# Kernel optimization log

Measured on AMD Instinct MI355X. Metric: run time of the kernel, lower is better.

Reference implementation:

```python
import jax, jax.numpy as jnp
import numpy as np

N, E, G = 51200, 819200, 256            # nodes, directed edges, graphs
N2, A, E2 = 102400, 204800, 409600      # 2-sets, assignments, 2-set edges
D, L, NI2, NAF = 64, 5, 36, 40          # emb_dim, num_layer, num_i_2, num_atom_features
EPS = 1e-5


def _seg_sum(v, seg, n):
    return jax.ops.segment_sum(v, seg, num_segments=n)


def _seg_mean(v, seg, n):
    s = jax.ops.segment_sum(v, seg, num_segments=n)
    c = jax.ops.segment_sum(jnp.ones((v.shape[0],), v.dtype), seg, num_segments=n)
    return s / jnp.maximum(c, 1.0)[:, None]


def setup_inputs() -> dict:
    key = jax.random.key(0)
    ks = iter(jax.random.split(key, 64))
    nrm = lambda shape: jax.random.normal(next(ks), shape, jnp.float32) * 0.1
    x = jax.random.normal(next(ks), (N, NAF), jnp.float32)
    edge_index = jax.random.randint(next(ks), (2, E), 0, N, dtype=jnp.int32)
    edge_attr = jnp.stack([jax.random.randint(next(ks), (E,), 0, 4, dtype=jnp.int32),
                           jax.random.randint(next(ks), (E,), 0, 3, dtype=jnp.int32)], axis=1)
    batch = jnp.repeat(jnp.arange(G, dtype=jnp.int32), N // G)
    iso_type_2 = jax.nn.one_hot(jax.random.randint(next(ks), (N2,), 0, NI2), NI2, dtype=jnp.float32)
    edge_index_2 = jax.random.randint(next(ks), (2, E2), 0, N2, dtype=jnp.int32)
    assignment_index_2 = jnp.stack([jax.random.randint(next(ks), (A,), 0, N, dtype=jnp.int32),
                                    jnp.repeat(jnp.arange(N2, dtype=jnp.int32), 2)], axis=0)
    batch_2 = jnp.repeat(jnp.arange(G, dtype=jnp.int32), N2 // G)
    params = dict(
        emb_W=nrm((NAF, D)), emb_b=jnp.zeros((D,), jnp.float32),
        gin_W1=nrm((L, D, 2 * D)), gin_b1=jnp.zeros((L, 2 * D), jnp.float32),
        gin_W2=nrm((L, 2 * D, D)), gin_b2=jnp.zeros((L, D), jnp.float32),
        eemb1=nrm((L, 6, D)), eemb2=nrm((L, 3, D)),
        bn_gamma=jnp.ones((L, D), jnp.float32), bn_beta=jnp.zeros((L, D), jnp.float32),
        iso1_rel_W=nrm((D + NI2, D)), iso1_rel_b=jnp.zeros((D,), jnp.float32),
        iso1_root_W=nrm((D + NI2, D)),
        iso2_rel_W=nrm((D, D)), iso2_rel_b=jnp.zeros((D,), jnp.float32),
        iso2_root_W=nrm((D, D)),
        ro_W0=nrm((2 * D, D)), ro_b0=jnp.zeros((D,), jnp.float32),
        ro_W1=nrm((D, D // 2)), ro_b1=jnp.zeros((D // 2,), jnp.float32),
        ro_W2=nrm((D // 2, D // 4)), ro_b2=jnp.zeros((D // 4,), jnp.float32),
        last_W=nrm((D // 4, 1)), last_b=jnp.zeros((1,), jnp.float32),
    )
    return dict(x=x, edge_index=edge_index, edge_attr=edge_attr, batch=batch,
                iso_type_2=iso_type_2, edge_index_2=edge_index_2,
                assignment_index_2=assignment_index_2, batch_2=batch_2, **params)


def _forward(x, iso_type_2, emb_W, emb_b, gin_W1, gin_b1, gin_W2, gin_b2,
             eemb1, eemb2, bn_gamma, bn_beta,
             iso1_rel_W, iso1_rel_b, iso1_root_W, iso2_rel_W, iso2_rel_b, iso2_root_W,
             ro_W0, ro_b0, ro_W1, ro_b1, ro_W2, ro_b2, last_W, last_b,
             edge_index, edge_attr, batch, edge_index_2, assignment_index_2, batch_2):
    # --- GIN stack with edge-feature embeddings and self loops ---
    loop = jnp.arange(N, dtype=edge_index.dtype)
    src = jnp.concatenate([edge_index[0], loop])
    dst = jnp.concatenate([edge_index[1], loop])
    sl_attr = jnp.tile(jnp.array([[4, 0]], dtype=edge_attr.dtype), (N, 1))
    ea = jnp.concatenate([edge_attr, sl_attr], axis=0)  # [E+N, 2]

    h = jax.nn.relu(x @ emb_W + emb_b)  # x_embedding1
    for l in range(L):
        e = eemb1[l][ea[:, 0]] + eemb2[l][ea[:, 1]]      # [E+N, D]
        agg = _seg_sum(h[src] + e, dst, N)               # gather + scatter-add
        h2 = jax.nn.relu(agg @ gin_W1[l] + gin_b1[l]) @ gin_W2[l] + gin_b2[l]
        mu = jnp.mean(h2, axis=0)
        var = jnp.var(h2, axis=0)                        # biased, torch BN training mode
        h2 = (h2 - mu) / jnp.sqrt(var + EPS) * bn_gamma[l] + bn_beta[l]
        h = h2 if l == L - 1 else jax.nn.relu(h2)        # last layer: no ReLU (JK='last')
    node_rep = h

    # --- graph mean pool of node representation ---
    x1 = _seg_mean(node_rep, batch, G)                   # [G, D]

    # --- 2-set branch: avg_pool onto 2-sets, concat iso type, two GraphConvs ---
    xp = _seg_mean(node_rep[assignment_index_2[0]], assignment_index_2[1], N2)
    xp = jnp.concatenate([xp, iso_type_2], axis=1)       # [N2, D+NI2]

    def graph_conv(z, Wrel, brel, Wroot):
        agg = _seg_sum(z[edge_index_2[0]], edge_index_2[1], N2)
        return agg @ Wrel + brel + z @ Wroot

    xp = jax.nn.relu(graph_conv(xp, iso1_rel_W, iso1_rel_b, iso1_root_W))
    xp = jax.nn.relu(graph_conv(xp, iso2_rel_W, iso2_rel_b, iso2_root_W))
    x2 = _seg_mean(xp, batch_2, G)                       # [G, D]

    # --- readout MLP ---
    m = jnp.concatenate([x1, x2], axis=1)                # [G, 2D]
    m = jax.nn.relu(m @ ro_W0 + ro_b0)
    m = jax.nn.relu(m @ ro_W1 + ro_b1)
    m = jax.nn.relu(m @ ro_W2 + ro_b2)
    m = m @ last_W + last_b
    return m.reshape(-1)                                 # num_tasks == 1 -> flat [G]


def reference(x, edge_index, edge_attr, batch, iso_type_2, edge_index_2,
              assignment_index_2, batch_2, emb_W, emb_b, gin_W1, gin_b1, gin_W2,
              gin_b2, eemb1, eemb2, bn_gamma, bn_beta, iso1_rel_W, iso1_rel_b,
              iso1_root_W, iso2_rel_W, iso2_rel_b, iso2_root_W, ro_W0, ro_b0,
              ro_W1, ro_b1, ro_W2, ro_b2, last_W, last_b):
    return _forward(x, iso_type_2, emb_W, emb_b, gin_W1, gin_b1, gin_W2, gin_b2,
                    eemb1, eemb2, bn_gamma, bn_beta,
                    iso1_rel_W, iso1_rel_b, iso1_root_W, iso2_rel_W, iso2_rel_b,
                    iso2_root_W, ro_W0, ro_b0, ro_W1, ro_b1, ro_W2, ro_b2,
                    last_W, last_b, edge_index, edge_attr, batch, edge_index_2,
                    assignment_index_2, batch_2)
```

## Files before the change

kernel.cpp:

```cpp
#include <hip/hip_runtime.h>

#define NN   51200
#define EE   819200
#define GG   256
#define NN2  102400
#define AA   204800
#define EE2  409600
#define DD   64
#define LL   5

#define NB1  100
#define NB2  200
#define CAP1 10240
#define CAP2 3072

typedef __attribute__((ext_vector_type(8))) short bf16x8;
typedef __attribute__((ext_vector_type(4))) float f32x4;
typedef unsigned short ushort_t;

#define OFF_H      ((size_t)0)
#define OFF_AGG    ((size_t)13107200)
#define OFF_H2     ((size_t)26214400)
#define OFF_XP     ((size_t)39321600)
#define OFF_REC1   OFF_XP
#define OFF_REC2   ((size_t)47513600)
#define OFF_PERM   ((size_t)60293120)
#define OFF_YROOT  ((size_t)65536000)
#define OFF_OFFS1  ((size_t)91750400)
#define OFF_COL1   ((size_t)91955216)
#define OFF_OFFS2  ((size_t)95232016)
#define OFF_COL2   ((size_t)95641632)
#define OFF_CNT1   ((size_t)97280032)
#define OFF_BBASE  ((size_t)97282080)
#define OFF_CUR1   ((size_t)97484832)
#define OFF_STATS  ((size_t)98508832)
#define ZERO_BYTES ((size_t)1231360)
#define OFF_ISO    ((size_t)98511392)
#define OFF_M      ((size_t)98920992)
#define WS_NEEDED  ((size_t)99052064)

__device__ __forceinline__ int waveInclScan(int v, int lane) {
#pragma unroll
    for (int off = 1; off < 64; off <<= 1) {
        int t = __shfl_up(v, off, 64);
        if (lane >= off) v += t;
    }
    return v;
}

__device__ __forceinline__ void bsplit(float x, ushort_t& hi, ushort_t& lo) {
    union { float f; unsigned u; } a; a.f = x;
    unsigned hb = (a.u + 0x7FFFu + ((a.u >> 16) & 1u)) >> 16;
    union { unsigned u; float f; } h; h.u = hb << 16;
    float r = x - h.f;
    union { float f; unsigned u; } b; b.f = r;
    unsigned lb = (b.u + 0x7FFFu + ((b.u >> 16) & 1u)) >> 16;
    hi = (ushort_t)hb; lo = (ushort_t)lb;
}

__global__ __launch_bounds__(256) void kbA(const int* __restrict__ src1, const int* __restrict__ dst1,
                                           const int* __restrict__ ea,
                                           const int* __restrict__ src2, const int* __restrict__ dst2,
                                           int* __restrict__ bucketCnt,
                                           int2* __restrict__ rec1, int2* __restrict__ rec2) {
    __shared__ int lhist[256];
    __shared__ int lbase[256];
    int tid = threadIdx.x, b = blockIdx.x;
    lhist[tid] = 0;
    __syncthreads();
    if (b < 400) {
        int i = (b * 256 + tid) * 8;
        int4 d0 = *(const int4*)(dst1 + i);
        int4 d1 = *(const int4*)(dst1 + i + 4);
        int dst[8] = {d0.x, d0.y, d0.z, d0.w, d1.x, d1.y, d1.z, d1.w};
        int bin[8], lr[8];
#pragma unroll
        for (int j = 0; j < 8; ++j) {
            bin[j] = dst[j] >> 9;
            lr[j] = atomicAdd(&lhist[bin[j]], 1);
        }
        __syncthreads();
        if (tid < NB1) {
            int c = lhist[tid];
            lbase[tid] = c ? atomicAdd(&bucketCnt[tid], c) : 0;
        }
        __syncthreads();
        int4 s0 = *(const int4*)(src1 + i);
        int4 s1 = *(const int4*)(src1 + i + 4);
        int src[8] = {s0.x, s0.y, s0.z, s0.w, s1.x, s1.y, s1.z, s1.w};
        int4 e0 = *(const int4*)(ea + 2 * i);
        int4 e1 = *(const int4*)(ea + 2 * i + 4);
        int4 e2 = *(const int4*)(ea + 2 * i + 8);
        int4 e3 = *(const int4*)(ea + 2 * i + 12);
        int code[8] = {e0.x * 3 + e0.y, e0.z * 3 + e0.w, e1.x * 3 + e1.y, e1.z * 3 + e1.w,
                       e2.x * 3 + e2.y, e2.z * 3 + e2.w, e3.x * 3 + e3.y, e3.z * 3 + e3.w};
#pragma unroll
        for (int j = 0; j < 8; ++j) {
            int pos = bin[j] * CAP1 + lbase[bin[j]] + lr[j];
            rec1[pos] = make_int2(src[j] | (code[j] << 16), dst[j]);
        }
    } else {
        int i = ((b - 400) * 256 + tid) * 8;
        int4 d0 = *(const int4*)(dst2 + i);
        int4 d1 = *(const int4*)(dst2 + i + 4);
        int dst[8] = {d0.x, d0.y, d0.z, d0.w, d1.x, d1.y, d1.z, d1.w};
        int bin[8], lr[8];
#pragma unroll
        for (int j = 0; j < 8; ++j) {
            bin[j] = dst[j] >> 9;
            lr[j] = atomicAdd(&lhist[bin[j]], 1);
        }
        __syncthreads();
        if (tid < NB2) {
            int c = lhist[tid];
            lbase[tid] = c ? atomicAdd(&bucketCnt[NB1 + tid], c) : 0;
        }
        __syncthreads();
        int4 s0 = *(const int4*)(src2 + i);
        int4 s1 = *(const int4*)(src2 + i + 4);
        int src[8] = {s0.x, s0.y, s0.z, s0.w, s1.x, s1.y, s1.z, s1.w};
#pragma unroll
        for (int j = 0; j < 8; ++j) {
            int pos = bin[j] * CAP2 + lbase[bin[j]] + lr[j];
            rec2[pos] = make_int2(src[j], dst[j]);
        }
    }
}

__global__ void kbscan(const int* __restrict__ bucketCnt, int* __restrict__ bucketBase) {
    __shared__ int wsum[4];
    int tid = threadIdx.x, lane = tid & 63, wid = tid >> 6;
    int nb = blockIdx.x ? NB2 : NB1;
    const int* cnt = bucketCnt + (blockIdx.x ? NB1 : 0);
    int* base = bucketBase + (blockIdx.x ? NB1 : 0);
    int v = (tid < nb) ? cnt[tid] : 0;
    int incl = waveInclScan(v, lane);
    if (lane == 63) wsum[wid] = incl;
    __syncthreads();
    int woff = 0;
#pragma unroll
    for (int w = 0; w < 3; ++w) woff += (w < wid) ? wsum[w] : 0;
    if (tid < nb) base[tid] = woff + incl - v;
}

__global__ __launch_bounds__(256) void kbB(const int* __restrict__ bucketCnt,
                                           const int* __restrict__ bucketBase,
                                           const int2* __restrict__ rec1, const int2* __restrict__ rec2,
                                           int* __restrict__ offs1, int* __restrict__ col1,
                                           int* __restrict__ offs2, int* __restrict__ col2,
                                           int* __restrict__ dbin) {
    __shared__ int nh[512];
    __shared__ int ncur[512];
    __shared__ int wsum[4];
    __shared__ int dhist[64];
    int tid = threadIdx.x, b = blockIdx.x;
    bool g1 = b < NB1;
    const int2* rec = g1 ? (rec1 + (size_t)b * CAP1) : (rec2 + (size_t)(b - NB1) * CAP2);
    int cnt = bucketCnt[b];
    int base = bucketBase[b];
    int* offs = g1 ? offs1 : offs2;
    int* col = g1 ? col1 : col2;
    int nodeBase = g1 ? b * 512 : (b - NB1) * 512;
    nh[tid] = 0; nh[tid + 256] = 0;
    if (tid < 64) dhist[tid] = 0;
    __syncthreads();
    for (int e = tid; e < cnt; e += 256) {
        int2 r = rec[e];
        atomicAdd(&nh[r.y & 511], 1);
    }
    __syncthreads();
    int v0 = nh[2 * tid], v1 = nh[2 * tid + 1];
    int s = v0 + v1;
    int lane = tid & 63, wid = tid >> 6;
    int incl = waveInclScan(s, lane);
    if (lane == 63) wsum[wid] = incl;
    __syncthreads();
    int woff = 0;
#pragma unroll
    for (int w = 0; w < 3; ++w) woff += (w < wid) ? wsum[w] : 0;
    int excl = woff + incl - s;
    ncur[2 * tid] = excl;
    ncur[2 * tid + 1] = excl + v0;
    offs[nodeBase + 2 * tid] = base + excl;
    offs[nodeBase + 2 * tid + 1] = base + excl + v0;
    if (g1) {
        atomicAdd(&dhist[v0 < 63 ? v0 : 63], 1);
        atomicAdd(&dhist[v1 < 63 ? v1 : 63], 1);
    }
    __syncthreads();
    for (int e = tid; e < cnt; e += 256) {
        int2 r = rec[e];
        int node = r.y & 511;
        int slot = base + atomicAdd(&ncur[node], 1);
        col[slot] = r.x;
    }
    if (g1 && tid < 64 && dhist[tid]) atomicAdd(&dbin[tid], dhist[tid]);
    if (tid == 0) {
        if (b == NB1 - 1) offs1[NN] = EE;
        if (b == NB1 + NB2 - 1) offs2[NN2] = EE2;
    }
}

__global__ void kprepx(const float* __restrict__ x, const float* __restrict__ embW,
                       const float* __restrict__ embB, float* __restrict__ h,
                       const float* __restrict__ gW1, const float* __restrict__ gW2,
                       ushort_t* __restrict__ w1h, ushort_t* __restrict__ w1l,
                       ushort_t* __restrict__ w2h, ushort_t* __restrict__ w2l,
                       const float* __restrict__ iso, int* __restrict__ isoIdx) {
    int b = blockIdx.x;
    if (b < 12800) {
        int t = b * 256 + threadIdx.x;
        int n = t >> 6, d = t & 63;
        float acc = embB[d];
        const float* xr = x + n * 40;
#pragma unroll
        for (int k = 0; k < 40; ++k) acc = fmaf(xr[k], embW[k * 64 + d], acc);
        h[(size_t)n * 64 + d] = fmaxf(acc, 0.f);
    } else if (b < 12840) {
        int t = (b - 12800) * 256 + threadIdx.x;
        int lane = t & 63, frag = t >> 6;
        int c15 = lane & 15, q = lane >> 4;
        if (frag < 80) {
            int kt = frag & 1, nt = (frag >> 1) & 7, l = frag >> 4;
            const float* W = gW1 + l * 8192;
            ushort_t* oh = w1h + ((size_t)frag * 64 + lane) * 8;
            ushort_t* ol = w1l + ((size_t)frag * 64 + lane) * 8;
            int kb = kt * 32 + q * 8, colw = nt * 16 + c15;
#pragma unroll
            for (int j = 0; j < 8; ++j) {
                ushort_t hi, lo; bsplit(W[(kb + j) * 128 + colw], hi, lo);
                oh[j] = hi; ol[j] = lo;
            }
        } else if (frag < 160) {
            int f = frag - 80;
            int kt = f & 3, nt = (f >> 2) & 3, l = f >> 4;
            const float* W = gW2 + l * 8192;
            ushort_t* oh = w2h + ((size_t)f * 64 + lane) * 8;
            ushort_t* ol = w2l + ((size_t)f * 64 + lane) * 8;
            int kb = kt * 32 + q * 8, colw = nt * 16 + c15;
#pragma unroll
            for (int j = 0; j < 8; ++j) {
                ushort_t hi, lo; bsplit(W[(kb + j) * 64 + colw], hi, lo);
                oh[j] = hi; ol[j] = lo;
            }
        }
    } else {
        int j = (b - 12840) * 256 + threadIdx.x;
        const float4* r4 = (const float4*)(iso + (size_t)j * 36);
        int best = 0;
#pragma unroll
        for (int k = 0; k < 9; ++k) {
            float4 v = r4[k];
            if (v.x > 0.5f) best = 4 * k;
            if (v.y > 0.5f) best = 4 * k + 1;
            if (v.z > 0.5f) best = 4 * k + 2;
            if (v.w > 0.5f) best = 4 * k + 3;
        }
        isoIdx[j] = best;
    }
}

__global__ void kdegscan(const int* __restrict__ dbin, int* __restrict__ dstart) {
    int tid = threadIdx.x;
    int v = dbin[tid];
    int incl = waveInclScan(v, tid);
    dstart[tid] = incl - v;
}

__global__ __launch_bounds__(256) void kdegplace(const int* __restrict__ offs,
                                                 const int* __restrict__ dstart,
                                                 int* __restrict__ dcur,
                                                 int* __restrict__ perm) {
    __shared__ int lhist[64];
    __shared__ int lbase[64];
    int tid = threadIdx.x;
    if (tid < 64) lhist[tid] = 0;
    __syncthreads();
    int n = blockIdx.x * 256 + tid;
    int d = offs[n + 1] - offs[n]; d = d < 63 ? d : 63;
    int lr = atomicAdd(&lhist[d], 1);
    __syncthreads();
    if (tid < 64) {
        int c = lhist[tid];
        lbase[tid] = c ? atomicAdd(&dcur[tid], c) : 0;
    }
    __syncthreads();
    perm[dstart[d] + lbase[d] + lr] = n;
}

__global__ __launch_bounds__(256) void ktrans(float* __restrict__ h,
                                              const float* __restrict__ pst,
                                              const float* __restrict__ gamma,
                                              const float* __restrict__ beta) {
    __shared__ float sstat[128];
    __shared__ float sSC[64], sSH[64];
    int tid = threadIdx.x;
    if (tid < 128) {
        float s = 0.f;
        const float* p = pst + tid;
#pragma unroll
        for (int i = 0; i < 32; ++i) s += p[i * 128];
        sstat[tid] = s;
    }
    __syncthreads();
    if (tid < 64) {
        float mu = sstat[tid] * (1.f / NN);
        float var = sstat[64 + tid] * (1.f / NN) - mu * mu;
        float sc = gamma[tid] * rsqrtf(var + 1e-5f);
        sSC[tid] = sc; sSH[tid] = beta[tid] - mu * sc;
    }
    __syncthreads();
    int c = (tid & 15) * 4;
    float4 sc4 = *(const float4*)(sSC + c);
    float4 sh4 = *(const float4*)(sSH + c);
    float4* hp = (float4*)h;
    size_t base = (size_t)blockIdx.x * 1024 + tid;
#pragma unroll
    for (int r = 0; r < 4; ++r) {
        float4 v = hp[base + r * 256];
        v.x = fmaxf(fmaf(v.x, sc4.x, sh4.x), 0.f);
        v.y = fmaxf(fmaf(v.y, sc4.y, sh4.y), 0.f);
        v.z = fmaxf(fmaf(v.z, sc4.z, sh4.z), 0.f);
        v.w = fmaxf(fmaf(v.w, sc4.w, sh4.w), 0.f);
        hp[base + r * 256] = v;
    }
}

__global__ __launch_bounds__(256) void kglayer(
    const float* __restrict__ hin, float* __restrict__ hout,
    const int* __restrict__ perm,
    const int* __restrict__ offs, const int* __restrict__ col,
    const float* __restrict__ e1, const float* __restrict__ e2,
    const ushort_t* __restrict__ w1h, const ushort_t* __restrict__ w1l,
    const ushort_t* __restrict__ w2h, const ushort_t* __restrict__ w2l,
    const float* __restrict__ b1, const float* __restrict__ b2,
    float* __restrict__ pstout) {
    __shared__ float etab[13 * 64];
    __shared__ int sPerm[16];
    __shared__ float sMLP[16 * 132];
    float* sA = sMLP;
    float* sH = sMLP;
    int tid = threadIdx.x;
    if (tid < 16) sPerm[tid] = perm[blockIdx.x * 16 + tid];
    for (int idx = tid; idx < 13 * 64; idx += 256) {
        int ci = idx >> 6, dd = idx & 63;
        etab[idx] = e1[(ci / 3) * 64 + dd] + e2[(ci % 3) * 64 + dd];
    }
    __syncthreads();
    int lane = tid & 63, wv = tid >> 6;
    int c15 = lane & 15, q = lane >> 4;

    {
        int n = sPerm[wv * 4 + q];
        int s0 = offs[n], s1 = offs[n + 1];
        float4 sx = *(const float4*)(hin + (size_t)n * 64 + 4 * c15);
        float4 et = *(const float4*)(etab + 12 * 64 + 4 * c15);
        float a0 = sx.x + et.x, a1 = sx.y + et.y, a2 = sx.z + et.z, a3 = sx.w + et.w;
        int deg = s1 - s0;
        if (deg > 0) {
            const int* cp = col + s0;
            int nfull = deg >> 3, rem = deg & 7;
            int vv[8];
#pragma unroll
            for (int j = 0; j < 8; ++j) {
                int idx = j < deg ? j : deg - 1;
                vv[j] = cp[idx];
            }
            for (int it = 0; it < nfull; ++it) {
                float4 xv[8], tv[8];
#pragma unroll
                for (int j = 0; j < 8; ++j) {
                    xv[j] = *(const float4*)(hin + (size_t)(vv[j] & 0xFFFF) * 64 + 4 * c15);
                    tv[j] = *(const float4*)(etab + (vv[j] >> 16) * 64 + 4 * c15);
                }
                int e8 = (it + 1) * 8;
                bool more = e8 < deg;
                int nx[8];
                if (more) {
#pragma unroll
                    for (int j = 0; j < 8; ++j) {
                        int idx = e8 + j; idx = idx < deg ? idx : deg - 1;
                        nx[j] = cp[idx];
                    }
                }
#pragma unroll
                for (int j = 0; j < 8; ++j) {
                    a0 += xv[j].x + tv[j].x;
                    a1 += xv[j].y + tv[j].y;
                    a2 += xv[j].z + tv[j].z;
                    a3 += xv[j].w + tv[j].w;
                }
                if (more) {
#pragma unroll
                    for (int j = 0; j < 8; ++j) vv[j] = nx[j];
                }
            }
            if (rem) {
                float4 xv[8], tv[8];
#pragma unroll
                for (int j = 0; j < 8; ++j) {
                    xv[j] = *(const float4*)(hin + (size_t)(vv[j] & 0xFFFF) * 64 + 4 * c15);
                    tv[j] = *(const float4*)(etab + (vv[j] >> 16) * 64 + 4 * c15);
                }
#pragma unroll
                for (int j = 0; j < 8; ++j) {
                    float mm = (j < rem) ? 1.f : 0.f;
                    a0 = fmaf(xv[j].x + tv[j].x, mm, a0);
                    a1 = fmaf(xv[j].y + tv[j].y, mm, a1);
                    a2 = fmaf(xv[j].z + tv[j].z, mm, a2);
                    a3 = fmaf(xv[j].w + tv[j].w, mm, a3);
                }
            }
        }
        *(float4*)(sA + (wv * 4 + q) * 68 + 4 * c15) = make_float4(a0, a1, a2, a3);
    }
    __syncthreads();

    bf16x8 ah[2], al[2];
#pragma unroll
    for (int kt = 0; kt < 2; ++kt) {
        const float* p = sA + c15 * 68 + kt * 32 + q * 8;
        float4 x0 = *(const float4*)p;
        float4 x1 = *(const float4*)(p + 4);
        float xs[8] = {x0.x, x0.y, x0.z, x0.w, x1.x, x1.y, x1.z, x1.w};
#pragma unroll
        for (int j = 0; j < 8; ++j) {
            ushort_t hi, lo; bsplit(xs[j], hi, lo);
            ah[kt][j] = (short)hi; al[kt][j] = (short)lo;
        }
    }
    __syncthreads();

    f32x4 acc1[2];
#pragma unroll
    for (int j = 0; j < 2; ++j) { f32x4 z = {0.f, 0.f, 0.f, 0.f}; acc1[j] = z; }
#pragma unroll
    for (int kt = 0; kt < 2; ++kt) {
#pragma unroll
        for (int j = 0; j < 2; ++j) {
            int nt = 2 * wv + j;
            size_t fo = ((size_t)((nt * 2 + kt) * 64 + lane)) * 8;
            bf16x8 bh = *(const bf16x8*)(w1h + fo);
            bf16x8 bl = *(const bf16x8*)(w1l + fo);
            acc1[j] = __builtin_amdgcn_mfma_f32_16x16x32_bf16(ah[kt], bh, acc1[j], 0, 0, 0);
            acc1[j] = __builtin_amdgcn_mfma_f32_16x16x32_bf16(al[kt], bh, acc1[j], 0, 0, 0);
            acc1[j] = __builtin_amdgcn_mfma_f32_16x16x32_bf16(ah[kt], bl, acc1[j], 0, 0, 0);
        }
    }
#pragma unroll
    for (int j = 0; j < 2; ++j) {
        int nt = 2 * wv + j;
        float bias = b1[nt * 16 + c15];
#pragma unroll
        for (int rg = 0; rg < 4; ++rg)
            sH[(4 * q + rg) * 132 + nt * 16 + c15] = fmaxf(acc1[j][rg] + bias, 0.f);
    }
    __syncthreads();

    f32x4 acc2 = {0.f, 0.f, 0.f, 0.f};
#pragma unroll
    for (int kt = 0; kt < 4; ++kt) {
        const float* p = sH + c15 * 132 + kt * 32 + q * 8;
        float4 x0 = *(const float4*)p;
        float4 x1 = *(const float4*)(p + 4);
        float xs[8] = {x0.x, x0.y, x0.z, x0.w, x1.x, x1.y, x1.z, x1.w};
        bf16x8 a2h, a2l;
#pragma unroll
        for (int j = 0; j < 8; ++j) {
            ushort_t hi, lo; bsplit(xs[j], hi, lo);
            a2h[j] = (short)hi; a2l[j] = (short)lo;
        }
        size_t fo = ((size_t)((wv * 4 + kt) * 64 + lane)) * 8;
        bf16x8 bh = *(const bf16x8*)(w2h + fo);
        bf16x8 bl = *(const bf16x8*)(w2l + fo);
        acc2 = __builtin_amdgcn_mfma_f32_16x16x32_bf16(a2h, bh, acc2, 0, 0, 0);
        acc2 = __builtin_amdgcn_mfma_f32_16x16x32_bf16(a2l, bh, acc2, 0, 0, 0);
        acc2 = __builtin_amdgcn_mfma_f32_16x16x32_bf16(a2h, bl, acc2, 0, 0, 0);
    }
    {
        float bias = b2[wv * 16 + c15];
        float s = 0.f, s2 = 0.f;
#pragma unroll
        for (int rg = 0; rg < 4; ++rg) {
            float v = acc2[rg] + bias;
            hout[(size_t)sPerm[4 * q + rg] * 64 + wv * 16 + c15] = v;
            s += v; s2 += v * v;
        }
        s += __shfl_xor(s, 16, 64);  s += __shfl_xor(s, 32, 64);
        s2 += __shfl_xor(s2, 16, 64); s2 += __shfl_xor(s2, 32, 64);
        if (q == 0) {
            float* ps = pstout + (size_t)(blockIdx.x & 31) * 128;
            atomicAdd(&ps[wv * 16 + c15], s);
            atomicAdd(&ps[64 + wv * 16 + c15], s2);
        }
    }
}

template <int FIRST>
__global__ __launch_bounds__(256) void kgcmm(const float* __restrict__ X,
                                             const float* __restrict__ Wrel,
                                             const float* __restrict__ Wroot,
                                             const float* __restrict__ WrelIso,
                                             const float* __restrict__ WrootIso,
                                             const int* __restrict__ isoIdx,
                                             float* __restrict__ Yrel,
                                             float* __restrict__ Yroot,
                                             const float* __restrict__ pst,
                                             const float* __restrict__ g4,
                                             const float* __restrict__ b4,
                                             const int* __restrict__ a0g,
                                             const float* __restrict__ h2src) {
    __shared__ float sX[64 * 65];
    __shared__ float sR[64 * 64];
    __shared__ float sT[64 * 64];
    __shared__ float sstat[128];
    __shared__ float sSC[64], sSH[64];
    int tid = threadIdx.x, blk = blockIdx.x;
    if (FIRST && tid < 128) {
        float s = 0.f;
        const float* p = pst + tid;
#pragma unroll
        for (int i = 0; i < 32; ++i) s += p[i * 128];
        sstat[tid] = s;
    }
#pragma unroll
    for (int i = tid; i < 1024; i += 256) {
        ((float4*)sR)[i] = ((const float4*)Wrel)[i];
        ((float4*)sT)[i] = ((const float4*)Wroot)[i];
    }
    __syncthreads();
    if (FIRST && tid < 64) {
        float mu = sstat[tid] * (1.f / NN);
        float var = sstat[64 + tid] * (1.f / NN) - mu * mu;
        float sc = g4[tid] * rsqrtf(var + 1e-5f);
        sSC[tid] = sc;
        sSH[tid] = b4[tid] - mu * sc;
    }
    __syncthreads();
#pragma unroll
    for (int i = tid; i < 1024; i += 256) {
        int row = i >> 4, c = (i & 15) << 2;
        float4 v;
        if (FIRST) {
            int grow = blk * 64 + row;
            int na = a0g[2 * grow], nb = a0g[2 * grow + 1];
            float4 va = *(const float4*)(h2src + (size_t)na * 64 + c);
            float4 vb = *(const float4*)(h2src + (size_t)nb * 64 + c);
            v.x = 0.5f * (va.x + vb.x); v.y = 0.5f * (va.y + vb.y);
            v.z = 0.5f * (va.z + vb.z); v.w = 0.5f * (va.w + vb.w);
            v.x = fmaf(v.x, sSC[c], sSH[c]);
            v.y = fmaf(v.y, sSC[c + 1], sSH[c + 1]);
            v.z = fmaf(v.z, sSC[c + 2], sSH[c + 2]);
            v.w = fmaf(v.w, sSC[c + 3], sSH[c + 3]);
        } else {
            v = ((const float4*)(X + (size_t)blk * 4096))[i];
        }
        float* p = sX + row * 65 + c;
        p[0] = v.x; p[1] = v.y; p[2] = v.z; p[3] = v.w;
    }
    __syncthreads();
    int tm = tid >> 4, tn = tid & 15;
    float aR[4][4], aT[4][4];
#pragma unroll
    for (int r = 0; r < 4; ++r)
#pragma unroll
        for (int c = 0; c < 4; ++c) { aR[r][c] = 0.f; aT[r][c] = 0.f; }
    const float* xrow = sX + tm * 4 * 65;
#pragma unroll 4
    for (int k = 0; k < 64; ++k) {
        float a0 = xrow[k], a1 = xrow[65 + k], a2 = xrow[130 + k], a3 = xrow[195 + k];
        float4 br = *(const float4*)(sR + k * 64 + tn * 4);
        float4 bt = *(const float4*)(sT + k * 64 + tn * 4);
        float rb[4] = {br.x, br.y, br.z, br.w};
        float tb[4] = {bt.x, bt.y, bt.z, bt.w};
#pragma unroll
        for (int c = 0; c < 4; ++c) {
            aR[0][c] = fmaf(a0, rb[c], aR[0][c]); aR[1][c] = fmaf(a1, rb[c], aR[1][c]);
            aR[2][c] = fmaf(a2, rb[c], aR[2][c]); aR[3][c] = fmaf(a3, rb[c], aR[3][c]);
            aT[0][c] = fmaf(a0, tb[c], aT[0][c]); aT[1][c] = fmaf(a1, tb[c], aT[1][c]);
            aT[2][c] = fmaf(a2, tb[c], aT[2][c]); aT[3][c] = fmaf(a3, tb[c], aT[3][c]);
        }
    }
#pragma unroll
    for (int r = 0; r < 4; ++r) {
        int row = blk * 64 + tm * 4 + r;
        float4 vr = make_float4(aR[r][0], aR[r][1], aR[r][2], aR[r][3]);
        float4 vt = make_float4(aT[r][0], aT[r][1], aT[r][2], aT[r][3]);
        if (FIRST) {
            int ii = isoIdx[row];
            float4 er = *(const float4*)(WrelIso + (size_t)ii * 64 + tn * 4);
            float4 et = *(const float4*)(WrootIso + (size_t)ii * 64 + tn * 4);
            vr.x += er.x; vr.y += er.y; vr.z += er.z; vr.w += er.w;
            vt.x += et.x; vt.y += et.y; vt.z += et.z; vt.w += et.w;
        }
        *(float4*)(Yrel + (size_t)row * 64 + tn * 4) = vr;
        *(float4*)(Yroot + (size_t)row * 64 + tn * 4) = vt;
    }
}

__global__ void kgather2(const float* __restrict__ yrel, const float* __restrict__ yroot,
                         const float* __restrict__ brel, const int* __restrict__ offs,
                         const int* __restrict__ col, float* __restrict__ out) {
    int t = blockIdx.x * 256 + threadIdx.x;
    int j = t >> 4, c = t & 15;
    int s0 = offs[j], s1 = offs[j + 1];
    float4 rt = *(const float4*)(yroot + (size_t)j * 64 + 4 * c);
    float4 bb = *(const float4*)(brel + 4 * c);
    float a0 = rt.x + bb.x, a1 = rt.y + bb.y, a2 = rt.z + bb.z, a3 = rt.w + bb.w;
    if (s0 < s1) {
        int vv[4];
#pragma unroll
        for (int jj = 0; jj < 4; ++jj) {
            int idx = s0 + jj; idx = idx < s1 ? idx : s1 - 1;
            vv[jj] = col[idx];
        }
        int e = s0;
        while (true) {
            int ne = e + 4;
            bool more = ne < s1;
            float4 xs[4];
#pragma unroll
            for (int jj = 0; jj < 4; ++jj)
                xs[jj] = *(const float4*)(yrel + (size_t)vv[jj] * 64 + 4 * c);
            int nx[4];
            if (more) {
#pragma unroll
                for (int jj = 0; jj < 4; ++jj) {
                    int idx = ne + jj; idx = idx < s1 ? idx : s1 - 1;
                    nx[jj] = col[idx];
                }
            }
#pragma unroll
            for (int jj = 0; jj < 4; ++jj) {
                float mm = (e + jj < s1) ? 1.f : 0.f;
                a0 = fmaf(xs[jj].x, mm, a0);
                a1 = fmaf(xs[jj].y, mm, a1);
                a2 = fmaf(xs[jj].z, mm, a2);
                a3 = fmaf(xs[jj].w, mm, a3);
            }
            if (!more) break;
            e = ne;
#pragma unroll
            for (int jj = 0; jj < 4; ++jj) vv[jj] = nx[jj];
        }
    }
    *(float4*)(out + (size_t)j * 64 + 4 * c) =
        make_float4(fmaxf(a0, 0.f), fmaxf(a1, 0.f), fmaxf(a2, 0.f), fmaxf(a3, 0.f));
}

__global__ void kpoolg(const float* __restrict__ h2, const float* __restrict__ xp2,
                       const float* __restrict__ pst, const float* __restrict__ g4,
                       const float* __restrict__ b4, float* __restrict__ m) {
    __shared__ float sstat[128];
    __shared__ float red[4][64];
    int g = blockIdx.x, tid = threadIdx.x;
    if (tid < 128) {
        float s = 0.f;
        const float* p = pst + tid;
#pragma unroll
        for (int i = 0; i < 32; ++i) s += p[i * 128];
        sstat[tid] = s;
    }
    int wid = tid >> 6, d = tid & 63;
    float s1 = 0.f;
    for (int i = wid; i < 200; i += 4) s1 += h2[((size_t)g * 200 + i) * 64 + d];
    red[wid][d] = s1;
    __syncthreads();
    if (wid == 0) {
        float mean = (red[0][d] + red[1][d] + red[2][d] + red[3][d]) * (1.f / 200.f);
        float mu = sstat[d] * (1.f / NN);
        float var = sstat[64 + d] * (1.f / NN) - mu * mu;
        float sc = g4[d] * rsqrtf(var + 1e-5f);
        m[g * 128 + d] = fmaf(mean, sc, b4[d] - mu * sc);
    }
    __syncthreads();
    float s2 = 0.f;
    for (int i = wid; i < 400; i += 4) s2 += xp2[((size_t)g * 400 + i) * 64 + d];
    red[wid][d] = s2;
    __syncthreads();
    if (wid == 0) m[g * 128 + 64 + d] = (red[0][d] + red[1][d] + red[2][d] + red[3][d]) * (1.f / 400.f);
}

__global__ void kread(const float* __restrict__ m, const float* __restrict__ W0,
                      const float* __restrict__ b0, const float* __restrict__ W1,
                      const float* __restrict__ b1, const float* __restrict__ W2,
                      const float* __restrict__ b2, const float* __restrict__ lw,
                      const float* __restrict__ lb, float* __restrict__ out) {
    __shared__ float s0[64], s1[32], s2[16];
    int g = blockIdx.x, d = threadIdx.x;
    const float* mr = m + g * 128;
    float t = b0[d];
    for (int k = 0; k < 128; ++k) t = fmaf(mr[k], W0[k * 64 + d], t);
    s0[d] = fmaxf(t, 0.f);
    __syncthreads();
    if (d < 32) {
        float u = b1[d];
        for (int k = 0; k < 64; ++k) u = fmaf(s0[k], W1[k * 32 + d], u);
        s1[d] = fmaxf(u, 0.f);
    }
    __syncthreads();
    if (d < 16) {
        float u = b2[d];
        for (int k = 0; k < 32; ++k) u = fmaf(s1[k], W2[k * 16 + d], u);
        s2[d] = fmaxf(u, 0.f);
    }
    __syncthreads();
    if (d == 0) {
        float u = lb[0];
        for (int k = 0; k < 16; ++k) u = fmaf(s2[k], lw[k], u);
        out[g] = u;
    }
}

extern "C" void kernel_launch(void* const* d_in, const int* in_sizes, int n_in,
                              void* d_out, int out_size, void* d_ws, size_t ws_size,
                              hipStream_t stream) {
    if (ws_size < WS_NEEDED) return;

    const float* x    = (const float*)d_in[0];
    const int*   ei   = (const int*)d_in[1];
    const int*   ea   = (const int*)d_in[2];
    const float* iso  = (const float*)d_in[4];
    const int*   ei2  = (const int*)d_in[5];
    const int*   ai2  = (const int*)d_in[6];
    const float* embW = (const float*)d_in[8];
    const float* embB = (const float*)d_in[9];
    const float* gW1  = (const float*)d_in[10];
    const float* gB1  = (const float*)d_in[11];
    const float* gW2  = (const float*)d_in[12];
    const float* gB2  = (const float*)d_in[13];
    const float* ee1  = (const float*)d_in[14];
    const float* ee2  = (const float*)d_in[15];
    const float* bng  = (const float*)d_in[16];
    const float* bnb  = (const float*)d_in[17];
    const float* i1rW = (const float*)d_in[18];
    const float* i1rB = (const float*)d_in[19];
    const float* i1tW = (const float*)d_in[20];
    const float* i2rW = (const float*)d_in[21];
    const float* i2rB = (const float*)d_in[22];
    const float* i2tW = (const float*)d_in[23];
    const float* roW0 = (const float*)d_in[24];
    const float* roB0 = (const float*)d_in[25];
    const float* roW1 = (const float*)d_in[26];
    const float* roB1 = (const float*)d_in[27];
    const float* roW2 = (const float*)d_in[28];
    const float* roB2 = (const float*)d_in[29];
    const float* lW   = (const float*)d_in[30];
    const float* lB   = (const float*)d_in[31];
    float* out = (float*)d_out;

    char* ws = (char*)d_ws;
    float* h      = (float*)(ws + OFF_H);
    float* hB     = (float*)(ws + OFF_AGG);
    float* hA     = (float*)(ws + OFF_H2);
    float* h2     = hA;
    float* xp     = (float*)(ws + OFF_XP);
    float* yrel   = (float*)(ws + OFF_H);
    float* yroot  = (float*)(ws + OFF_YROOT);
    int* offs1    = (int*)(ws + OFF_OFFS1);
    int* col1     = (int*)(ws + OFF_COL1);
    int* offs2    = (int*)(ws + OFF_OFFS2);
    int* col2     = (int*)(ws + OFF_COL2);
    int* isoIdx   = (int*)(ws + OFF_ISO);
    float* mbuf   = (float*)(ws + OFF_M);
    ushort_t* w1h = (ushort_t*)(ws + OFF_YROOT);
    ushort_t* w1l = (ushort_t*)(ws + OFF_YROOT + 81920);
    ushort_t* w2h = (ushort_t*)(ws + OFF_YROOT + 163840);
    ushort_t* w2l = (ushort_t*)(ws + OFF_YROOT + 245760);
    float* pstat2 = (float*)(ws + OFF_CUR1);
    int2* rec1    = (int2*)(ws + OFF_REC1);
    int2* rec2    = (int2*)(ws + OFF_REC2);
    int* bucketCnt  = (int*)(ws + OFF_CNT1);
    int* bucketBase = (int*)(ws + OFF_BBASE);
    int* perm     = (int*)(ws + OFF_PERM);
    int* dbin     = (int*)(ws + OFF_STATS);
    int* dstart   = dbin + 64;
    int* dcur     = dbin + 128;

    const int* src1 = ei;
    const int* dst1 = ei + EE;
    const int* src2 = ei2;
    const int* dst2 = ei2 + EE2;
    const int* a0   = ai2;

    hipMemsetAsync(ws + OFF_CNT1, 0, ZERO_BYTES, stream);

    kbA<<<600, 256, 0, stream>>>(src1, dst1, ea, src2, dst2, bucketCnt, rec1, rec2);
    kprepx<<<13240, 256, 0, stream>>>(x, embW, embB, h, gW1, gW2,
                                      w1h, w1l, w2h, w2l, iso, isoIdx);
    kbscan<<<2, 256, 0, stream>>>(bucketCnt, bucketBase);
    kbB<<<300, 256, 0, stream>>>(bucketCnt, bucketBase, rec1, rec2,
                                 offs1, col1, offs2, col2, dbin);
    kdegscan<<<1, 64, 0, stream>>>(dbin, dstart);
    kdegplace<<<NN / 256, 256, 0, stream>>>(offs1, dstart, dcur, perm);

    for (int l = 0; l < LL; ++l) {
        const float* hin = (l == 0) ? h : ((l & 1) ? hA : hB);
        float* hout = (l & 1) ? hB : hA;
        kglayer<<<NN / 16, 256, 0, stream>>>(
            hin, hout, perm, offs1, col1, ee1 + l * 384, ee2 + l * 192,
            w1h + (size_t)l * 8192, w1l + (size_t)l * 8192,
            w2h + (size_t)l * 8192, w2l + (size_t)l * 8192,
            gB1 + l * 128, gB2 + l * 64,
            pstat2 + (size_t)l * 4096);
        if (l < LL - 1)
            ktrans<<<800, 256, 0, stream>>>(hout, pstat2 + (size_t)l * 4096,
                                            bng + l * 64, bnb + l * 64);
    }

    kgcmm<1><<<NN2 / 64, 256, 0, stream>>>(xp, i1rW, i1tW, i1rW + 64 * 64,
                                           i1tW + 64 * 64, isoIdx, yrel, yroot,
                                           pstat2 + (size_t)4 * 4096,
                                           bng + 4 * 64, bnb + 4 * 64, a0, h2);
    kgather2<<<NN2 * 16 / 256, 256, 0, stream>>>(yrel, yroot, i1rB, offs2, col2, xp);
    kgcmm<0><<<NN2 / 64, 256, 0, stream>>>(xp, i2rW, i2tW, nullptr, nullptr,
                                           nullptr, yrel, yroot,
                                           nullptr, nullptr, nullptr, nullptr, nullptr);
    kgather2<<<NN2 * 16 / 256, 256, 0, stream>>>(yrel, yroot, i2rB, offs2, col2, xp);

    kpoolg<<<GG, 256, 0, stream>>>(h2, xp, pstat2 + (size_t)4 * 4096,
                                   bng + 4 * 64, bnb + 4 * 64, mbuf);
    kread<<<GG, 64, 0, stream>>>(mbuf, roW0, roB0, roW1, roB1, roW2, roB2, lW, lB, out);
}
```

Before: 591.5 us.

## Use split-bf16 MFMA for graph-conv matmuls and split iso-index kernel

Replaces the scalar FP32 shared-memory matmul in kgcmm with MFMA 16x16x32 bf16 instructions, using a hi/lo split (three products) to keep near-FP32 accuracy. Weights are pre-split into MFMA fragment layout inside kprepx. The iso argmax moves to its own kernel that stages rows through shared memory for coalesced loads. The embedding loop now uses float4 loads. This trades scalar FMA work and the per-block weight staging for extra prep work and strided output stores.

```diff
diff --git a/kernel.cpp b/kernel.cpp
--- a/kernel.cpp
+++ b/kernel.cpp
@@ -201,20 +201,44 @@
     }
 }
 
+__global__ __launch_bounds__(256) void kiso(const float* __restrict__ iso, int* __restrict__ isoIdx) {
+    __shared__ float srow[256 * 36];
+    int tid = threadIdx.x;
+    int base = blockIdx.x * 256;
+    const float4* g4p = (const float4*)(iso + (size_t)base * 36);
+#pragma unroll
+    for (int i = tid; i < 2304; i += 256) ((float4*)srow)[i] = g4p[i];
+    __syncthreads();
+    const float* r = srow + tid * 36;
+    int best = 0;
+#pragma unroll
+    for (int k = 0; k < 36; ++k)
+        if (r[k] > 0.5f) best = k;
+    isoIdx[base + tid] = best;
+}
+
 __global__ void kprepx(const float* __restrict__ x, const float* __restrict__ embW,
                        const float* __restrict__ embB, float* __restrict__ h,
                        const float* __restrict__ gW1, const float* __restrict__ gW2,
                        ushort_t* __restrict__ w1h, ushort_t* __restrict__ w1l,
                        ushort_t* __restrict__ w2h, ushort_t* __restrict__ w2l,
-                       const float* __restrict__ iso, int* __restrict__ isoIdx) {
+                       const float* __restrict__ i1rW, const float* __restrict__ i1tW,
+                       const float* __restrict__ i2rW, const float* __restrict__ i2tW,
+                       ushort_t* __restrict__ gcwh, ushort_t* __restrict__ gcwl) {
     int b = blockIdx.x;
     if (b < 12800) {
         int t = b * 256 + threadIdx.x;
         int n = t >> 6, d = t & 63;
         float acc = embB[d];
-        const float* xr = x + n * 40;
-#pragma unroll
-        for (int k = 0; k < 40; ++k) acc = fmaf(xr[k], embW[k * 64 + d], acc);
+        const float4* xr4 = (const float4*)(x + (size_t)n * 40);
+#pragma unroll
+        for (int k4 = 0; k4 < 10; ++k4) {
+            float4 xv = xr4[k4];
+            acc = fmaf(xv.x, embW[(4 * k4 + 0) * 64 + d], acc);
+            acc = fmaf(xv.y, embW[(4 * k4 + 1) * 64 + d], acc);
+            acc = fmaf(xv.z, embW[(4 * k4 + 2) * 64 + d], acc);
+            acc = fmaf(xv.w, embW[(4 * k4 + 3) * 64 + d], acc);
+        }
         h[(size_t)n * 64 + d] = fmaxf(acc, 0.f);
     } else if (b < 12840) {
         int t = (b - 12800) * 256 + threadIdx.x;
@@ -245,18 +269,20 @@
             }
         }
     } else {
-        int j = (b - 12840) * 256 + threadIdx.x;
-        const float4* r4 = (const float4*)(iso + (size_t)j * 36);
-        int best = 0;
-#pragma unroll
-        for (int k = 0; k < 9; ++k) {
-            float4 v = r4[k];
-            if (v.x > 0.5f) best = 4 * k;
-            if (v.y > 0.5f) best = 4 * k + 1;
-            if (v.z > 0.5f) best = 4 * k + 2;
-            if (v.w > 0.5f) best = 4 * k + 3;
-        }
-        isoIdx[j] = best;
+        int t = (b - 12840) * 256 + threadIdx.x;
+        int lane = t & 63, frag = t >> 6;
+        int c15 = lane & 15, q = lane >> 4;
+        int m = frag >> 3, f = frag & 7;
+        int kt = f & 1, nt = f >> 1;
+        const float* W = (m == 0) ? i1rW : (m == 1) ? i1tW : (m == 2) ? i2rW : i2tW;
+        ushort_t* oh = gcwh + (size_t)m * 4096 + ((size_t)f * 64 + lane) * 8;
+        ushort_t* ol = gcwl + (size_t)m * 4096 + ((size_t)f * 64 + lane) * 8;
+        int kb = kt * 32 + q * 8, colw = nt * 16 + c15;
+#pragma unroll
+        for (int j = 0; j < 8; ++j) {
+            ushort_t hi, lo; bsplit(W[(kb + j) * 64 + colw], hi, lo);
+            oh[j] = hi; ol[j] = lo;
+        }
     }
 }
 
@@ -498,8 +524,10 @@
 
 template <int FIRST>
 __global__ __launch_bounds__(256) void kgcmm(const float* __restrict__ X,
-                                             const float* __restrict__ Wrel,
-                                             const float* __restrict__ Wroot,
+                                             const ushort_t* __restrict__ grh,
+                                             const ushort_t* __restrict__ grl,
+                                             const ushort_t* __restrict__ gth,
+                                             const ushort_t* __restrict__ gtl,
                                              const float* __restrict__ WrelIso,
                                              const float* __restrict__ WrootIso,
                                              const int* __restrict__ isoIdx,
@@ -510,9 +538,7 @@
                                              const float* __restrict__ b4,
                                              const int* __restrict__ a0g,
                                              const float* __restrict__ h2src) {
-    __shared__ float sX[64 * 65];
-    __shared__ float sR[64 * 64];
-    __shared__ float sT[64 * 64];
+    __shared__ float sX[64 * 68];
     __shared__ float sstat[128];
     __shared__ float sSC[64], sSH[64];
     int tid = threadIdx.x, blk = blockIdx.x;
@@ -522,11 +548,6 @@
 #pragma unroll
         for (int i = 0; i < 32; ++i) s += p[i * 128];
         sstat[tid] = s;
-    }
-#pragma unroll
-    for (int i = tid; i < 1024; i += 256) {
-        ((float4*)sR)[i] = ((const float4*)Wrel)[i];
-        ((float4*)sT)[i] = ((const float4*)Wroot)[i];
     }
     __syncthreads();
     if (FIRST && tid < 64) {
@@ -555,46 +576,68 @@
         } else {
             v = ((const float4*)(X + (size_t)blk * 4096))[i];
         }
-        float* p = sX + row * 65 + c;
+        float* p = sX + row * 68 + c;
         p[0] = v.x; p[1] = v.y; p[2] = v.z; p[3] = v.w;
     }
     __syncthreads();
-    int tm = tid >> 4, tn = tid & 15;
-    float aR[4][4], aT[4][4];
-#pragma unroll
-    for (int r = 0; r < 4; ++r)
-#pragma unroll
-        for (int c = 0; c < 4; ++c) { aR[r][c] = 0.f; aT[r][c] = 0.f; }
-    const float* xrow = sX + tm * 4 * 65;
-#pragma unroll 4
-    for (int k = 0; k < 64; ++k) {
-        float a0 = xrow[k], a1 = xrow[65 + k], a2 = xrow[130 + k], a3 = xrow[195 + k];
-        float4 br = *(const float4*)(sR + k * 64 + tn * 4);
-        float4 bt = *(const float4*)(sT + k * 64 + tn * 4);
-        float rb[4] = {br.x, br.y, br.z, br.w};
-        float tb[4] = {bt.x, bt.y, bt.z, bt.w};
-#pragma unroll
-        for (int c = 0; c < 4; ++c) {
-            aR[0][c] = fmaf(a0, rb[c], aR[0][c]); aR[1][c] = fmaf(a1, rb[c], aR[1][c]);
-            aR[2][c] = fmaf(a2, rb[c], aR[2][c]); aR[3][c] = fmaf(a3, rb[c], aR[3][c]);
-            aT[0][c] = fmaf(a0, tb[c], aT[0][c]); aT[1][c] = fmaf(a1, tb[c], aT[1][c]);
-            aT[2][c] = fmaf(a2, tb[c], aT[2][c]); aT[3][c] = fmaf(a3, tb[c], aT[3][c]);
-        }
-    }
-#pragma unroll
-    for (int r = 0; r < 4; ++r) {
-        int row = blk * 64 + tm * 4 + r;
-        float4 vr = make_float4(aR[r][0], aR[r][1], aR[r][2], aR[r][3]);
-        float4 vt = make_float4(aT[r][0], aT[r][1], aT[r][2], aT[r][3]);
-        if (FIRST) {
-            int ii = isoIdx[row];
-            float4 er = *(const float4*)(WrelIso + (size_t)ii * 64 + tn * 4);
-            float4 et = *(const float4*)(WrootIso + (size_t)ii * 64 + tn * 4);
-            vr.x += er.x; vr.y += er.y; vr.z += er.z; vr.w += er.w;
-            vt.x += et.x; vt.y += et.y; vt.z += et.z; vt.w += et.w;
-        }
-        *(float4*)(Yrel + (size_t)row * 64 + tn * 4) = vr;
-        *(float4*)(Yroot + (size_t)row * 64 + tn * 4) = vt;
+    int lane = tid & 63, wv = tid >> 6;
+    int c15 = lane & 15, q = lane >> 4;
+
+    bf16x8 ah[2], al[2];
+#pragma unroll
+    for (int kt = 0; kt < 2; ++kt) {
+        const float* p = sX + (16 * wv + c15) * 68 + kt * 32 + q * 8;
+        float4 x0 = *(const float4*)p;
+        float4 x1 = *(const float4*)(p + 4);
+        float xs[8] = {x0.x, x0.y, x0.z, x0.w, x1.x, x1.y, x1.z, x1.w};
+#pragma unroll
+        for (int j = 0; j < 8; ++j) {
+            ushort_t hi, lo; bsplit(xs[j], hi, lo);
+            ah[kt][j] = (short)hi; al[kt][j] = (short)lo;
+        }
+    }
+
+    f32x4 accR[4], accT[4];
+#pragma unroll
+    for (int nt = 0; nt < 4; ++nt) {
+        f32x4 z = {0.f, 0.f, 0.f, 0.f};
+        accR[nt] = z; accT[nt] = z;
+    }
+#pragma unroll
+    for (int nt = 0; nt < 4; ++nt) {
+#pragma unroll
+        for (int kt = 0; kt < 2; ++kt) {
+            size_t fo = ((size_t)((nt * 2 + kt) * 64 + lane)) * 8;
+            bf16x8 bh = *(const bf16x8*)(grh + fo);
+            bf16x8 bl = *(const bf16x8*)(grl + fo);
+            accR[nt] = __builtin_amdgcn_mfma_f32_16x16x32_bf16(ah[kt], bh, accR[nt], 0, 0, 0);
+            accR[nt] = __builtin_amdgcn_mfma_f32_16x16x32_bf16(al[kt], bh, accR[nt], 0, 0, 0);
+            accR[nt] = __builtin_amdgcn_mfma_f32_16x16x32_bf16(ah[kt], bl, accR[nt], 0, 0, 0);
+            bf16x8 ch = *(const bf16x8*)(gth + fo);
+            bf16x8 cl = *(const bf16x8*)(gtl + fo);
+            accT[nt] = __builtin_amdgcn_mfma_f32_16x16x32_bf16(ah[kt], ch, accT[nt], 0, 0, 0);
+            accT[nt] = __builtin_amdgcn_mfma_f32_16x16x32_bf16(al[kt], ch, accT[nt], 0, 0, 0);
+            accT[nt] = __builtin_amdgcn_mfma_f32_16x16x32_bf16(ah[kt], cl, accT[nt], 0, 0, 0);
+        }
+    }
+
+    int rbase = blk * 64 + 16 * wv + 4 * q;
+#pragma unroll
+    for (int rg = 0; rg < 4; ++rg) {
+        int row = rbase + rg;
+        int ii = FIRST ? isoIdx[row] : 0;
+        float* yr = Yrel + (size_t)row * 64;
+        float* yt = Yroot + (size_t)row * 64;
+        const float* er = WrelIso + (size_t)ii * 64;
+        const float* et = WrootIso + (size_t)ii * 64;
+#pragma unroll
+        for (int nt = 0; nt < 4; ++nt) {
+            int cc = nt * 16 + c15;
+            float vr = accR[nt][rg], vt = accT[nt][rg];
+            if (FIRST) { vr += er[cc]; vt += et[cc]; }
+            yr[cc] = vr;
+            yt[cc] = vt;
+        }
     }
 }
 
@@ -767,6 +810,8 @@
     ushort_t* w1l = (ushort_t*)(ws + OFF_YROOT + 81920);
     ushort_t* w2h = (ushort_t*)(ws + OFF_YROOT + 163840);
     ushort_t* w2l = (ushort_t*)(ws + OFF_YROOT + 245760);
+    ushort_t* gcwh = (ushort_t*)(ws + OFF_M);
+    ushort_t* gcwl = (ushort_t*)(ws + OFF_M + 32768);
     float* pstat2 = (float*)(ws + OFF_CUR1);
     int2* rec1    = (int2*)(ws + OFF_REC1);
     int2* rec2    = (int2*)(ws + OFF_REC2);
@@ -786,8 +831,10 @@
     hipMemsetAsync(ws + OFF_CNT1, 0, ZERO_BYTES, stream);
 
     kbA<<<600, 256, 0, stream>>>(src1, dst1, ea, src2, dst2, bucketCnt, rec1, rec2);
-    kprepx<<<13240, 256, 0, stream>>>(x, embW, embB, h, gW1, gW2,
-                                      w1h, w1l, w2h, w2l, iso, isoIdx);
+    kiso<<<NN2 / 256, 256, 0, stream>>>(iso, isoIdx);
+    kprepx<<<12848, 256, 0, stream>>>(x, embW, embB, h, gW1, gW2,
+                                      w1h, w1l, w2h, w2l,
+                                      i1rW, i1tW, i2rW, i2tW, gcwh, gcwl);
     kbscan<<<2, 256, 0, stream>>>(bucketCnt, bucketBase);
     kbB<<<300, 256, 0, stream>>>(bucketCnt, bucketBase, rec1, rec2,
                                  offs1, col1, offs2, col2, dbin);
@@ -808,13 +855,17 @@
                                             bng + l * 64, bnb + l * 64);
     }
 
-    kgcmm<1><<<NN2 / 64, 256, 0, stream>>>(xp, i1rW, i1tW, i1rW + 64 * 64,
-                                           i1tW + 64 * 64, isoIdx, yrel, yroot,
+    kgcmm<1><<<NN2 / 64, 256, 0, stream>>>(xp,
+                                           gcwh, gcwl, gcwh + 4096, gcwl + 4096,
+                                           i1rW + 64 * 64, i1tW + 64 * 64, isoIdx,
+                                           yrel, yroot,
                                            pstat2 + (size_t)4 * 4096,
                                            bng + 4 * 64, bnb + 4 * 64, a0, h2);
     kgather2<<<NN2 * 16 / 256, 256, 0, stream>>>(yrel, yroot, i1rB, offs2, col2, xp);
-    kgcmm<0><<<NN2 / 64, 256, 0, stream>>>(xp, i2rW, i2tW, nullptr, nullptr,
-                                           nullptr, yrel, yroot,
+    kgcmm<0><<<NN2 / 64, 256, 0, stream>>>(xp,
+                                           gcwh + 8192, gcwl + 8192, gcwh + 12288, gcwl + 12288,
+                                           nullptr, nullptr, nullptr,
+                                           yrel, yroot,
                                            nullptr, nullptr, nullptr, nullptr, nullptr);
     kgather2<<<NN2 * 16 / 256, 256, 0, stream>>>(yrel, yroot, i2rB, offs2, col2, xp);
 
```

Measured after the change: 572.1 us. -3.3%, faster.
